# Kernel optimization log

Hardware: AMD Instinct MI355X
Metric: run time of the kernel (lower is better)

The kernel has to match this reference:

```python
import jax, jax.numpy as jnp
import numpy as np

NUM_INPUTS = 256
L1, L2 = 256, 128
NUM_ACTIONS = 17
NUM_EXPERTS = 4
GATE_H = 32
BATCH = 131072


def setup_inputs() -> dict:
    key = jax.random.key(0)
    ks = jax.random.split(key, 16)
    s = 0.05
    return {
        "x": jax.random.normal(ks[0], (BATCH, NUM_INPUTS), jnp.float32),
        # stacked expert weights [E, in, out]
        "W1": jax.random.normal(ks[1], (NUM_EXPERTS, NUM_INPUTS, L1), jnp.float32) * s,
        "b1": jax.random.normal(ks[2], (NUM_EXPERTS, L1), jnp.float32) * s,
        "W2": jax.random.normal(ks[3], (NUM_EXPERTS, L1, L2), jnp.float32) * s,
        "b2": jax.random.normal(ks[4], (NUM_EXPERTS, L2), jnp.float32) * s,
        "Wmu": jax.random.normal(ks[5], (NUM_EXPERTS, L2, NUM_ACTIONS), jnp.float32) * s,
        "bmu": jax.random.normal(ks[6], (NUM_EXPERTS, NUM_ACTIONS), jnp.float32) * s,
        # gate (BlendingModule) params
        "gW1": jax.random.normal(ks[7], (NUM_INPUTS, GATE_H), jnp.float32) * s,
        "gb1": jax.random.normal(ks[8], (GATE_H,), jnp.float32) * s,
        "gW2": jax.random.normal(ks[9], (GATE_H, GATE_H), jnp.float32) * s,
        "gb2": jax.random.normal(ks[10], (GATE_H,), jnp.float32) * s,
        "gWo": jax.random.normal(ks[11], (GATE_H, NUM_EXPERTS), jnp.float32) * s,
        "gbo": jax.random.normal(ks[12], (NUM_EXPERTS,), jnp.float32) * s,
    }


def _gate(x, gW1, gb1, gW2, gb2, gWo, gbo):
    h = jax.nn.elu(x @ gW1 + gb1)
    h = jax.nn.elu(h @ gW2 + gb2)
    return jax.nn.softmax(h @ gWo + gbo, axis=1)  # [B, E]


def reference(x, W1, b1, W2, b2, Wmu, bmu, gW1, gb1, gW2, gb2, gWo, gbo):
    coeffs = _gate(x, gW1, gb1, gW2, gb2, gWo, gbo)  # [B, E]
    # layer 1: gate-weighted sum of 4 expert GEMMs, then ReLU
    h = jnp.einsum("bi,eio->beo", x, W1) + b1[None]          # [B, E, L1]
    h = jax.nn.relu(jnp.einsum("be,beo->bo", coeffs, h))     # [B, L1]
    # layer 2
    h = jnp.einsum("bi,eio->beo", h, W2) + b2[None]          # [B, E, L2]
    h = jax.nn.relu(jnp.einsum("be,beo->bo", coeffs, h))     # [B, L2]
    # output head: weighted sum, no activation
    mu = jnp.einsum("bi,eio->beo", h, Wmu) + bmu[None]       # [B, E, A]
    mu = jnp.einsum("be,beo->bo", coeffs, mu)                # [B, A]
    return mu
```

## Files before the change

kernel.cpp:

```cpp
#include <hip/hip_runtime.h>


typedef _Float16 half8 __attribute__((ext_vector_type(8)));
typedef _Float16 half4v __attribute__((ext_vector_type(4)));
typedef float floatx4 __attribute__((ext_vector_type(4)));

#define MFMA16(a, b, c) __builtin_amdgcn_mfma_f32_16x16x32_f16(a, b, c, 0, 0, 0)
#define WAIT_VM(N) asm volatile("s_waitcnt vmcnt(" #N ")" ::: "memory")
#define WAIT_LGKM0 asm volatile("s_waitcnt lgkmcnt(0)" ::: "memory")

__device__ __forceinline__ void barrier_mem() {
  asm volatile("" ::: "memory");
  __builtin_amdgcn_s_barrier();
  asm volatile("" ::: "memory");
}

__device__ __forceinline__ half8 splat8(_Float16 v) {
  half8 r = {v, v, v, v, v, v, v, v};
  return r;
}

__device__ __forceinline__ void load_lds16(const _Float16* g, _Float16* s) {
  __builtin_amdgcn_global_load_lds((__attribute__((address_space(1))) void*)(g),
                                   (__attribute__((address_space(3))) void*)(s), 16, 0, 0);
}

enum {
  W1P = 0,
  W2P = 262144,
  WMUP = 393216,
  GW1P = 409600,
  GW2P = 417792,
  B1P = 418816,
  B2P = 427008,
  BMUP = 431104,
  WS_TOTAL = 432128
};

__global__ __launch_bounds__(256) void prep_kernel(
    const float* __restrict__ W1, const float* __restrict__ W2,
    const float* __restrict__ Wmu, const float* __restrict__ gW1,
    const float* __restrict__ gW2, const float* __restrict__ b1,
    const float* __restrict__ b2, const float* __restrict__ bmu,
    _Float16* __restrict__ ws) {
  int p = blockIdx.x * 256 + threadIdx.x;
  if (p >= WS_TOTAL) return;
  float v = 0.f;
  if (p < W2P) {
    int q = p, ks = q >> 13, r = q & 8191, ct = r >> 9, l = (r >> 3) & 63, j = r & 7;
    int k = ks * 32 + ((l >> 4) << 3) + j, o = (ct << 4) + (l & 15);
    v = W1[k * 256 + o];
  } else if (p < WMUP) {
    int q = p - W2P, ks = q >> 12, r = q & 4095, ct = r >> 9, l = (r >> 3) & 63, j = r & 7;
    int k = ks * 32 + ((l >> 4) << 3) + j, o = (ct << 4) + (l & 15);
    v = W2[k * 128 + o];
  } else if (p < GW1P) {
    int q = p - WMUP, ks = q >> 10, r = q & 1023, ct = r >> 9, l = (r >> 3) & 63, j = r & 7;
    int k = ks * 32 + ((l >> 4) << 3) + j, o = (ct << 4) + (l & 15);
    v = (o < 17) ? Wmu[k * 17 + o] : 0.f;
  } else if (p < GW2P) {
    int q = p - GW1P, ks = q >> 10, r = q & 1023, ct = r >> 9, l = (r >> 3) & 63, j = r & 7;
    int k = ks * 32 + ((l >> 4) << 3) + j, o = (ct << 4) + (l & 15);
    v = gW1[k * 32 + o];
  } else if (p < B1P) {
    int q = p - GW2P, ct = q >> 9, l = (q >> 3) & 63, j = q & 7;
    int k = ((l >> 4) << 3) + j, o = (ct << 4) + (l & 15);
    v = gW2[k * 32 + o];
  } else if (p < B2P) {
    int q = p - B1P, ct = q >> 9, l = (q >> 3) & 63, j = q & 7;
    int k = ((l >> 4) << 3) + j, o = (ct << 4) + (l & 15);
    v = (k < 4) ? b1[k * 256 + o] : 0.f;
  } else if (p < BMUP) {
    int q = p - B2P, ct = q >> 9, l = (q >> 3) & 63, j = q & 7;
    int k = ((l >> 4) << 3) + j, o = (ct << 4) + (l & 15);
    v = (k < 4) ? b2[k * 128 + o] : 0.f;
  } else {
    int q = p - BMUP, ct = q >> 9, l = (q >> 3) & 63, j = q & 7;
    int k = ((l >> 4) << 3) + j, o = (ct << 4) + (l & 15);
    v = (k < 4 && o < 17) ? bmu[k * 17 + o] : 0.f;
  }
  ws[p] = (_Float16)v;
}

enum { XS = 264, X_HW = 128 * XS, STG_HW = 3 * 8192, CP_OFF = X_HW + STG_HW, LDS_HW = CP_OFF + 128 * 32 };

__global__ __launch_bounds__(512, 2) void actor_kernel(
    const float* __restrict__ x, const _Float16* __restrict__ ws,
    const float* __restrict__ gb1, const float* __restrict__ gb2,
    const float* __restrict__ gWo, const float* __restrict__ gbo,
    float* __restrict__ out) {
  __shared__ __align__(16) _Float16 lds[LDS_HW];
  _Float16* xl = lds;
  _Float16* stg = lds + X_HW;
  _Float16* cp = lds + CP_OFF;

  const int tid = threadIdx.x;
  const int l = tid & 63;
  const int w = tid >> 6;
  const int l15 = l & 15;
  const int g8 = (l >> 4) << 3;
  const int wrow16 = w * 16;
  const int wr = (w >> 2) * 64;
  const int wc1 = (w & 3) * 64;
  const int wc2 = (w & 3) * 32;
  const long rowbase = (long)blockIdx.x * 128;

  {
    const float* xp = x + rowbase * 256;
#pragma unroll 4
    for (int it = 0; it < 16; ++it) {
      int row = w + it * 8;
      int c4 = (l)*4;
      float4 v = *(const float4*)(xp + row * 256 + c4);
      half4v h = {(_Float16)v.x, (_Float16)v.y, (_Float16)v.z, (_Float16)v.w};
      *(half4v*)(&xl[row * XS + c4]) = h;
    }
    for (int i = w; i < 16; i += 8) load_lds16(ws + GW1P + i * 512 + l * 8, stg + i * 512);
    for (int i = w; i < 2; i += 8) load_lds16(ws + GW2P + i * 512 + l * 8, stg + 8192 + i * 512);
    WAIT_VM(0);
    WAIT_LGKM0;
    barrier_mem();
  }

  {
    const floatx4 z4 = {0.f, 0.f, 0.f, 0.f};
    floatx4 ga[2] = {z4, z4};
#pragma unroll
    for (int ks = 0; ks < 8; ++ks) {
      half8 a = *(const half8*)(&xl[(wrow16 + l15) * XS + ks * 32 + g8]);
#pragma unroll
      for (int ct = 0; ct < 2; ++ct) {
        half8 b = *(const half8*)(&stg[ks * 1024 + ct * 512 + l * 8]);
        ga[ct] = MFMA16(a, b, ga[ct]);
      }
    }
#pragma unroll
    for (int ct = 0; ct < 2; ++ct) {
      int col = ct * 16 + l15;
      float bias = gb1[col];
#pragma unroll
      for (int rg = 0; rg < 4; ++rg) {
        int row = wrow16 + ((l >> 4) << 2) + rg;
        float v = ga[ct][rg] + bias;
        v = (v > 0.f) ? v : (__expf(v) - 1.f);
        stg[16384 + row * 40 + col] = (_Float16)v;
      }
    }
    WAIT_LGKM0;
    barrier_mem();
  }

  {
    const floatx4 z4 = {0.f, 0.f, 0.f, 0.f};
    floatx4 ga[2] = {z4, z4};
    half8 a = *(const half8*)(&stg[16384 + (wrow16 + l15) * 40 + g8]);
#pragma unroll
    for (int ct = 0; ct < 2; ++ct) {
      half8 b = *(const half8*)(&stg[8192 + ct * 512 + l * 8]);
      ga[ct] = MFMA16(a, b, ga[ct]);
    }
#pragma unroll
    for (int ct = 0; ct < 2; ++ct) {
      int col = ct * 16 + l15;
      float bias = gb2[col];
#pragma unroll
      for (int rg = 0; rg < 4; ++rg) {
        int row = wrow16 + ((l >> 4) << 2) + rg;
        float v = ga[ct][rg] + bias;
        v = (v > 0.f) ? v : (__expf(v) - 1.f);
        stg[row * 40 + col] = (_Float16)v;
      }
    }
    WAIT_LGKM0;
    barrier_mem();
  }

  {
    int row = tid >> 2, e = tid & 3;
    float s = gbo[e];
#pragma unroll
    for (int i8 = 0; i8 < 4; ++i8) {
      half8 gv = *(const half8*)(&stg[row * 40 + i8 * 8]);
#pragma unroll
      for (int j = 0; j < 8; ++j) s += (float)gv[j] * gWo[(i8 * 8 + j) * 4 + e];
    }
    ((float*)(stg + 8192))[row * 4 + e] = s;
    WAIT_LGKM0;
    barrier_mem();
  }

  if (tid < 128) {
    const float* lg = (const float*)(stg + 8192) + tid * 4;
    float m0 = fmaxf(fmaxf(lg[0], lg[1]), fmaxf(lg[2], lg[3]));
    float e0 = __expf(lg[0] - m0), e1 = __expf(lg[1] - m0);
    float e2 = __expf(lg[2] - m0), e3 = __expf(lg[3] - m0);
    float inv = 1.f / (e0 + e1 + e2 + e3);
    _Float16* cr = &cp[tid * 32];
    cr[0] = (_Float16)(e0 * inv);
    cr[1] = (_Float16)(e1 * inv);
    cr[2] = (_Float16)(e2 * inv);
    cr[3] = (_Float16)(e3 * inv);
#pragma unroll
    for (int z = 4; z < 32; ++z) cr[z] = (_Float16)0.f;
  }
  for (int i = w; i < 16; i += 8) load_lds16(ws + B1P + i * 512 + l * 8, stg + i * 512);
  WAIT_LGKM0;
  barrier_mem();

  _Float16 c16[4][4];
#pragma unroll
  for (int rt = 0; rt < 4; ++rt)
#pragma unroll
    for (int e = 0; e < 4; ++e) c16[rt][e] = cp[(wr + rt * 16 + l15) * 32 + e];
  for (int i = w; i < 16; i += 8) load_lds16(ws + W1P + i * 512 + l * 8, stg + 8192 + i * 512);
  WAIT_VM(2);
  barrier_mem();

  floatx4 acc[4][4];
  {
    const floatx4 z4 = {0.f, 0.f, 0.f, 0.f};
#pragma unroll
    for (int rt = 0; rt < 4; ++rt) {
      half8 a = *(const half8*)(&cp[(wr + rt * 16 + l15) * 32 + g8]);
#pragma unroll
      for (int ct = 0; ct < 4; ++ct) {
        half8 b = *(const half8*)(&stg[((w & 3) * 4 + ct) * 512 + l * 8]);
        acc[rt][ct] = MFMA16(a, b, z4);
      }
    }
  }
  for (int i = w; i < 16; i += 8) load_lds16(ws + W1P + 8192 + i * 512 + l * 8, stg + 16384 + i * 512);

#pragma unroll
  for (int e = 0; e < 4; ++e) {
    const half8 cs[4] = {splat8(c16[0][e]), splat8(c16[1][e]), splat8(c16[2][e]), splat8(c16[3][e])};
#pragma unroll 1
    for (int t8 = 0; t8 < 8; ++t8) {
      const int t = e * 8 + t8 + 1;
      if (t == 32) { WAIT_VM(0); } else { WAIT_VM(2); }
      barrier_mem();
      const int xk = t8 << 5;
      const _Float16* bb = stg + (t % 3) * 8192;
      half8 a[4];
#pragma unroll
      for (int rt = 0; rt < 4; ++rt) {
        half8 raw = *(const half8*)(&xl[(wr + rt * 16 + l15) * XS + xk + g8]);
        a[rt] = raw * cs[rt];
      }
#pragma unroll
      for (int ct = 0; ct < 4; ++ct) {
        half8 b = *(const half8*)(&bb[((w & 3) * 4 + ct) * 512 + l * 8]);
#pragma unroll
        for (int rt = 0; rt < 4; ++rt) acc[rt][ct] = MFMA16(a[rt], b, acc[rt][ct]);
      }
      if (t <= 30) {
        const _Float16* src = ws + W1P + (t + 1) * 8192;
        _Float16* dst = stg + ((t + 2) % 3) * 8192;
        for (int i = w; i < 16; i += 8) load_lds16(src + i * 512 + l * 8, dst + i * 512);
      }
    }
  }
  barrier_mem();

#pragma unroll
  for (int rt = 0; rt < 4; ++rt)
#pragma unroll
    for (int ct = 0; ct < 4; ++ct) {
      int col = wc1 + ct * 16 + l15;
#pragma unroll
      for (int rg = 0; rg < 4; ++rg) {
        int row = wr + rt * 16 + ((l >> 4) << 2) + rg;
        float v = acc[rt][ct][rg];
        xl[row * XS + col] = (_Float16)(v > 0.f ? v : 0.f);
      }
    }
  for (int i = w; i < 8; i += 8) load_lds16(ws + B2P + i * 512 + l * 8, stg + i * 512);
  WAIT_LGKM0;
  barrier_mem();
  for (int i = w; i < 8; i += 8) load_lds16(ws + W2P + i * 512 + l * 8, stg + 8192 + i * 512);
  WAIT_VM(1);
  barrier_mem();

  floatx4 acc2[4][2];
  {
    const floatx4 z4 = {0.f, 0.f, 0.f, 0.f};
#pragma unroll
    for (int rt = 0; rt < 4; ++rt) {
      half8 a = *(const half8*)(&cp[(wr + rt * 16 + l15) * 32 + g8]);
#pragma unroll
      for (int ct = 0; ct < 2; ++ct) {
        half8 b = *(const half8*)(&stg[((w & 3) * 2 + ct) * 512 + l * 8]);
        acc2[rt][ct] = MFMA16(a, b, z4);
      }
    }
  }
  for (int i = w; i < 8; i += 8) load_lds16(ws + W2P + 4096 + i * 512 + l * 8, stg + 16384 + i * 512);

#pragma unroll
  for (int e = 0; e < 4; ++e) {
    const half8 cs[4] = {splat8(c16[0][e]), splat8(c16[1][e]), splat8(c16[2][e]), splat8(c16[3][e])};
#pragma unroll 1
    for (int t8 = 0; t8 < 8; ++t8) {
      const int t = e * 8 + t8 + 1;
      if (t == 32) { WAIT_VM(0); } else { WAIT_VM(1); }
      barrier_mem();
      const int xk = t8 << 5;
      const _Float16* bb = stg + (t % 3) * 8192;
      half8 a[4];
#pragma unroll
      for (int rt = 0; rt < 4; ++rt) {
        half8 raw = *(const half8*)(&xl[(wr + rt * 16 + l15) * XS + xk + g8]);
        a[rt] = raw * cs[rt];
      }
#pragma unroll
      for (int ct = 0; ct < 2; ++ct) {
        half8 b = *(const half8*)(&bb[((w & 3) * 2 + ct) * 512 + l * 8]);
#pragma unroll
        for (int rt = 0; rt < 4; ++rt) acc2[rt][ct] = MFMA16(a[rt], b, acc2[rt][ct]);
      }
      if (t <= 30) {
        const _Float16* src = ws + W2P + (t + 1) * 4096;
        _Float16* dst = stg + ((t + 2) % 3) * 8192;
        for (int i = w; i < 8; i += 8) load_lds16(src + i * 512 + l * 8, dst + i * 512);
      }
    }
  }
  barrier_mem();

#pragma unroll
  for (int rt = 0; rt < 4; ++rt)
#pragma unroll
    for (int ct = 0; ct < 2; ++ct) {
      int col = wc2 + ct * 16 + l15;
#pragma unroll
      for (int rg = 0; rg < 4; ++rg) {
        int row = wr + rt * 16 + ((l >> 4) << 2) + rg;
        float v = acc2[rt][ct][rg];
        xl[row * 136 + col] = (_Float16)(v > 0.f ? v : 0.f);
      }
    }
  for (int i = w; i < 34; i += 8) {
    int tile = i >> 1, half = i & 1;
    const _Float16* src = ws + (tile == 0 ? BMUP : WMUP + (tile - 1) * 1024) + half * 512 + l * 8;
    load_lds16(src, stg + i * 512);
  }
  WAIT_LGKM0;
  WAIT_VM(0);
  barrier_mem();

  floatx4 hacc[2];
  {
    const floatx4 z4 = {0.f, 0.f, 0.f, 0.f};
    half8 a = *(const half8*)(&cp[(wrow16 + l15) * 32 + g8]);
#pragma unroll
    for (int ct = 0; ct < 2; ++ct) {
      half8 b = *(const half8*)(&stg[ct * 512 + l * 8]);
      hacc[ct] = MFMA16(a, b, z4);
    }
  }
#pragma unroll
  for (int ksv = 0; ksv < 16; ++ksv) {
    const int e = ksv >> 2;
    const int xk = (ksv & 3) << 5;
    half8 raw = *(const half8*)(&xl[(wrow16 + l15) * 136 + xk + g8]);
    half8 a = raw * splat8(c16[w & 3][e]);
#pragma unroll
    for (int ct = 0; ct < 2; ++ct) {
      half8 b = *(const half8*)(&stg[(ksv + 1) * 1024 + ct * 512 + l * 8]);
      hacc[ct] = MFMA16(a, b, hacc[ct]);
    }
  }
#pragma unroll
  for (int ct = 0; ct < 2; ++ct) {
    int col = ct * 16 + l15;
    if (col < 17) {
#pragma unroll
      for (int rg = 0; rg < 4; ++rg) {
        int row = wrow16 + ((l >> 4) << 2) + rg;
        out[(rowbase + row) * 17 + col] = hacc[ct][rg];
      }
    }
  }
}

extern "C" void kernel_launch(void* const* d_in, const int* in_sizes, int n_in,
                              void* d_out, int out_size, void* d_ws, size_t ws_size,
                              hipStream_t stream) {
  const float* x = (const float*)d_in[0];
  const float* W1 = (const float*)d_in[1];
  const float* b1 = (const float*)d_in[2];
  const float* W2 = (const float*)d_in[3];
  const float* b2 = (const float*)d_in[4];
  const float* Wmu = (const float*)d_in[5];
  const float* bmu = (const float*)d_in[6];
  const float* gW1 = (const float*)d_in[7];
  const float* gb1 = (const float*)d_in[8];
  const float* gW2 = (const float*)d_in[9];
  const float* gb2 = (const float*)d_in[10];
  const float* gWo = (const float*)d_in[11];
  const float* gbo = (const float*)d_in[12];
  float* out = (float*)d_out;
  _Float16* ws = (_Float16*)d_ws;

  prep_kernel<<<(WS_TOTAL + 255) / 256, 256, 0, stream>>>(W1, W2, Wmu, gW1, gW2, b1, b2, bmu, ws);
  actor_kernel<<<1024, 512, 0, stream>>>(x, ws, gb1, gb2, gWo, gbo, out);
}
```

Measured before the change: 354.3 us.

## Rewrite actor kernel with 1024-thread blocks, fragment-layout LDS and deeper weight ring

Restructures the fused MoE actor kernel to use 16 waves per block arranged as 2 row groups by 8 column groups. Activations are stored in LDS in MFMA fragment order, removing the padded row-major layout. The gate output projection moves onto MFMA with shuffle-based softmax. Weight tiles stream through a deeper 5-slot ring for layer 1 and a 10-slot ring for layer 2, with the prep kernel reordering weights to match. The aim is to raise MFMA occupancy, cut LDS bank conflicts and hide weight-load latency. In exchange only one wave group computes the gate, and barriers now synchronize 16 waves.

Result: slower. 1.139 ms (+221.5%).

```diff
diff --git a/kernel.cpp b/kernel.cpp
--- a/kernel.cpp
+++ b/kernel.cpp
@@ -18,6 +18,13 @@
 __device__ __forceinline__ half8 splat8(_Float16 v) {
   half8 r = {v, v, v, v, v, v, v, v};
   return r;
+}
+
+__device__ __forceinline__ half8 make_cfrag(half4v c, int l) {
+  half8 cf = {(_Float16)0, (_Float16)0, (_Float16)0, (_Float16)0,
+              (_Float16)0, (_Float16)0, (_Float16)0, (_Float16)0};
+  if (l < 16) { cf[0] = c[0]; cf[1] = c[1]; cf[2] = c[2]; cf[3] = c[3]; }
+  return cf;
 }
 
 __device__ __forceinline__ void load_lds16(const _Float16* g, _Float16* s) {
@@ -31,354 +38,396 @@
   WMUP = 393216,
   GW1P = 409600,
   GW2P = 417792,
-  B1P = 418816,
-  B2P = 427008,
-  BMUP = 431104,
-  WS_TOTAL = 432128
+  GWOP = 418816,
+  B1P = 419328,
+  B2P = 427520,
+  BMUP = 431616,
+  WS_TOTAL = 432640
 };
 
 __global__ __launch_bounds__(256) void prep_kernel(
     const float* __restrict__ W1, const float* __restrict__ W2,
     const float* __restrict__ Wmu, const float* __restrict__ gW1,
-    const float* __restrict__ gW2, const float* __restrict__ b1,
-    const float* __restrict__ b2, const float* __restrict__ bmu,
-    _Float16* __restrict__ ws) {
+    const float* __restrict__ gW2, const float* __restrict__ gWo,
+    const float* __restrict__ b1, const float* __restrict__ b2,
+    const float* __restrict__ bmu, _Float16* __restrict__ ws) {
   int p = blockIdx.x * 256 + threadIdx.x;
   if (p >= WS_TOTAL) return;
   float v = 0.f;
   if (p < W2P) {
-    int q = p, ks = q >> 13, r = q & 8191, ct = r >> 9, l = (r >> 3) & 63, j = r & 7;
-    int k = ks * 32 + ((l >> 4) << 3) + j, o = (ct << 4) + (l & 15);
-    v = W1[k * 256 + o];
+    int t = p >> 13, r = p & 8191;
+    int ct = r >> 9, l = (r >> 3) & 63, j = r & 7;
+    int o = ct * 16 + (l & 15), krel = ((l >> 4) << 3) + j;
+    int t8 = t >> 2, e = t & 3;
+    v = W1[(e * 256 + t8 * 32 + krel) * 256 + o];
   } else if (p < WMUP) {
-    int q = p - W2P, ks = q >> 12, r = q & 4095, ct = r >> 9, l = (r >> 3) & 63, j = r & 7;
-    int k = ks * 32 + ((l >> 4) << 3) + j, o = (ct << 4) + (l & 15);
-    v = W2[k * 128 + o];
+    int q = p - W2P, t = q >> 12, r = q & 4095;
+    int ct = r >> 9, l = (r >> 3) & 63, j = r & 7;
+    int o = ct * 16 + (l & 15), krel = ((l >> 4) << 3) + j;
+    int t8 = t >> 2, e = t & 3;
+    v = W2[(e * 256 + t8 * 32 + krel) * 128 + o];
   } else if (p < GW1P) {
-    int q = p - WMUP, ks = q >> 10, r = q & 1023, ct = r >> 9, l = (r >> 3) & 63, j = r & 7;
-    int k = ks * 32 + ((l >> 4) << 3) + j, o = (ct << 4) + (l & 15);
-    v = (o < 17) ? Wmu[k * 17 + o] : 0.f;
+    int q = p - WMUP, t = q >> 10, r = q & 1023;
+    int ct = r >> 9, l = (r >> 3) & 63, j = r & 7;
+    int o = ct * 16 + (l & 15), krel = ((l >> 4) << 3) + j;
+    int t2 = t >> 2, e = t & 3;
+    v = (o < 17) ? Wmu[(e * 128 + t2 * 32 + krel) * 17 + o] : 0.f;
   } else if (p < GW2P) {
-    int q = p - GW1P, ks = q >> 10, r = q & 1023, ct = r >> 9, l = (r >> 3) & 63, j = r & 7;
-    int k = ks * 32 + ((l >> 4) << 3) + j, o = (ct << 4) + (l & 15);
-    v = gW1[k * 32 + o];
+    int q = p - GW1P, ks = q >> 10, r = q & 1023;
+    int ct = r >> 9, l = (r >> 3) & 63, j = r & 7;
+    int o = ct * 16 + (l & 15), krel = ((l >> 4) << 3) + j;
+    v = gW1[(ks * 32 + krel) * 32 + o];
+  } else if (p < GWOP) {
+    int q = p - GW2P;
+    int ct = q >> 9, l = (q >> 3) & 63, j = q & 7;
+    int o = ct * 16 + (l & 15), krel = ((l >> 4) << 3) + j;
+    v = gW2[krel * 32 + o];
   } else if (p < B1P) {
-    int q = p - GW2P, ct = q >> 9, l = (q >> 3) & 63, j = q & 7;
-    int k = ((l >> 4) << 3) + j, o = (ct << 4) + (l & 15);
-    v = gW2[k * 32 + o];
+    int q = p - GWOP;
+    int l = (q >> 3) & 63, j = q & 7;
+    int o = l & 15, krel = ((l >> 4) << 3) + j;
+    v = (o < 4) ? gWo[krel * 4 + o] : 0.f;
   } else if (p < B2P) {
-    int q = p - B1P, ct = q >> 9, l = (q >> 3) & 63, j = q & 7;
-    int k = ((l >> 4) << 3) + j, o = (ct << 4) + (l & 15);
-    v = (k < 4) ? b1[k * 256 + o] : 0.f;
+    int q = p - B1P;
+    int ct = q >> 9, l = (q >> 3) & 63, j = q & 7;
+    int o = ct * 16 + (l & 15), krel = ((l >> 4) << 3) + j;
+    v = (krel < 4) ? b1[krel * 256 + o] : 0.f;
   } else if (p < BMUP) {
-    int q = p - B2P, ct = q >> 9, l = (q >> 3) & 63, j = q & 7;
-    int k = ((l >> 4) << 3) + j, o = (ct << 4) + (l & 15);
-    v = (k < 4) ? b2[k * 128 + o] : 0.f;
+    int q = p - B2P;
+    int ct = q >> 9, l = (q >> 3) & 63, j = q & 7;
+    int o = ct * 16 + (l & 15), krel = ((l >> 4) << 3) + j;
+    v = (krel < 4) ? b2[krel * 128 + o] : 0.f;
   } else {
-    int q = p - BMUP, ct = q >> 9, l = (q >> 3) & 63, j = q & 7;
-    int k = ((l >> 4) << 3) + j, o = (ct << 4) + (l & 15);
-    v = (k < 4 && o < 17) ? bmu[k * 17 + o] : 0.f;
+    int q = p - BMUP;
+    int ct = q >> 9, l = (q >> 3) & 63, j = q & 7;
+    int o = ct * 16 + (l & 15), krel = ((l >> 4) << 3) + j;
+    v = (krel < 4 && o < 17) ? bmu[krel * 17 + o] : 0.f;
   }
   ws[p] = (_Float16)v;
 }
 
-enum { XS = 264, X_HW = 128 * XS, STG_HW = 3 * 8192, CP_OFF = X_HW + STG_HW, LDS_HW = CP_OFF + 128 * 32 };
-
-__global__ __launch_bounds__(512, 2) void actor_kernel(
+enum {
+  RING = 32768,
+  GATE = 57344,
+  GW2L = GATE + 8192,
+  GWOL = GATE + 9216,
+  BNC = GATE + 9728,
+  CLDS = GATE + 13824,
+  LDS_HW = 73728
+};
+
+__global__ __launch_bounds__(1024, 4) void actor_kernel(
     const float* __restrict__ x, const _Float16* __restrict__ ws,
     const float* __restrict__ gb1, const float* __restrict__ gb2,
-    const float* __restrict__ gWo, const float* __restrict__ gbo,
-    float* __restrict__ out) {
+    const float* __restrict__ gbo, float* __restrict__ out) {
   __shared__ __align__(16) _Float16 lds[LDS_HW];
-  _Float16* xl = lds;
-  _Float16* stg = lds + X_HW;
-  _Float16* cp = lds + CP_OFF;
-
   const int tid = threadIdx.x;
   const int l = tid & 63;
   const int w = tid >> 6;
   const int l15 = l & 15;
   const int g8 = (l >> 4) << 3;
-  const int wrow16 = w * 16;
-  const int wr = (w >> 2) * 64;
-  const int wc1 = (w & 3) * 64;
-  const int wc2 = (w & 3) * 32;
+  const int mr = w >> 3;
+  const int nc = w & 7;
   const long rowbase = (long)blockIdx.x * 128;
+  const int fragBase = mr * 2048 + l * 8;
+  const floatx4 z4 = {0.f, 0.f, 0.f, 0.f};
 
   {
-    const float* xp = x + rowbase * 256;
-#pragma unroll 4
-    for (int it = 0; it < 16; ++it) {
-      int row = w + it * 8;
-      int c4 = (l)*4;
-      float4 v = *(const float4*)(xp + row * 256 + c4);
-      half4v h = {(_Float16)v.x, (_Float16)v.y, (_Float16)v.z, (_Float16)v.w};
-      *(half4v*)(&xl[row * XS + c4]) = h;
-    }
-    for (int i = w; i < 16; i += 8) load_lds16(ws + GW1P + i * 512 + l * 8, stg + i * 512);
-    for (int i = w; i < 2; i += 8) load_lds16(ws + GW2P + i * 512 + l * 8, stg + 8192 + i * 512);
-    WAIT_VM(0);
+    const float* xp = x + (rowbase + mr * 64) * 256 + nc * 32 + g8;
+#pragma unroll
+    for (int rt = 0; rt < 4; ++rt) {
+      const float4* rp = (const float4*)(xp + (rt * 16 + l15) * 256);
+      float4 v0 = rp[0], v1 = rp[1];
+      half8 h = {(_Float16)v0.x, (_Float16)v0.y, (_Float16)v0.z, (_Float16)v0.w,
+                 (_Float16)v1.x, (_Float16)v1.y, (_Float16)v1.z, (_Float16)v1.w};
+      *(half8*)(&lds[nc * 4096 + fragBase + rt * 512]) = h;
+    }
+    for (int c = w; c < 19; c += 16)
+      load_lds16(ws + GW1P + c * 512 + l * 8, lds + GATE + c * 512);
+#pragma unroll
+    for (int t = 0; t < 3; ++t)
+      load_lds16(ws + (t == 0 ? B1P : W1P + (t - 1) * 8192) + w * 512 + l * 8,
+                 lds + RING + t * 8192 + w * 512);
+    WAIT_VM(3);
     WAIT_LGKM0;
     barrier_mem();
   }
 
+  if (nc == 0) {
+    floatx4 ga[4][2];
+#pragma unroll
+    for (int rt = 0; rt < 4; ++rt) { ga[rt][0] = z4; ga[rt][1] = z4; }
+#pragma unroll
+    for (int ks = 0; ks < 8; ++ks) {
+      half8 b0 = *(const half8*)(&lds[GATE + ks * 1024 + l * 8]);
+      half8 b1v = *(const half8*)(&lds[GATE + ks * 1024 + 512 + l * 8]);
+#pragma unroll
+      for (int rt = 0; rt < 4; ++rt) {
+        half8 a = *(const half8*)(&lds[ks * 4096 + fragBase + rt * 512]);
+        ga[rt][0] = MFMA16(a, b0, ga[rt][0]);
+        ga[rt][1] = MFMA16(a, b1v, ga[rt][1]);
+      }
+    }
+#pragma unroll
+    for (int rt = 0; rt < 4; ++rt)
+#pragma unroll
+      for (int ct = 0; ct < 2; ++ct) {
+        const int c32 = ct * 16 + l15;
+        const float bias = gb1[c32];
+        const int hi4 = (c32 >> 3) << 4, jj = c32 & 7;
+#pragma unroll
+        for (int rg = 0; rg < 4; ++rg) {
+          float vv = ga[rt][ct][rg] + bias;
+          vv = vv > 0.f ? vv : (__expf(vv) - 1.f);
+          const int lp = (4 * (l >> 4) + rg) | hi4;
+          lds[BNC + mr * 2048 + rt * 512 + lp * 8 + jj] = (_Float16)vv;
+        }
+      }
+    WAIT_LGKM0;
+    floatx4 g2[4][2];
+    {
+      half8 bw0 = *(const half8*)(&lds[GW2L + l * 8]);
+      half8 bw1 = *(const half8*)(&lds[GW2L + 512 + l * 8]);
+#pragma unroll
+      for (int rt = 0; rt < 4; ++rt) {
+        half8 a = *(const half8*)(&lds[BNC + mr * 2048 + rt * 512 + l * 8]);
+        g2[rt][0] = MFMA16(a, bw0, z4);
+        g2[rt][1] = MFMA16(a, bw1, z4);
+      }
+    }
+    WAIT_LGKM0;
+#pragma unroll
+    for (int rt = 0; rt < 4; ++rt)
+#pragma unroll
+      for (int ct = 0; ct < 2; ++ct) {
+        const int c32 = ct * 16 + l15;
+        const float bias = gb2[c32];
+        const int hi4 = (c32 >> 3) << 4, jj = c32 & 7;
+#pragma unroll
+        for (int rg = 0; rg < 4; ++rg) {
+          float vv = g2[rt][ct][rg] + bias;
+          vv = vv > 0.f ? vv : (__expf(vv) - 1.f);
+          const int lp = (4 * (l >> 4) + rg) | hi4;
+          lds[BNC + mr * 2048 + rt * 512 + lp * 8 + jj] = (_Float16)vv;
+        }
+      }
+    WAIT_LGKM0;
+    {
+      half8 bo = *(const half8*)(&lds[GWOL + l * 8]);
+      const float bze = (l15 < 4) ? gbo[l15] : 0.f;
+#pragma unroll
+      for (int rt = 0; rt < 4; ++rt) {
+        half8 a = *(const half8*)(&lds[BNC + mr * 2048 + rt * 512 + l * 8]);
+        floatx4 lg = MFMA16(a, bo, z4);
+#pragma unroll
+        for (int rg = 0; rg < 4; ++rg) {
+          float vv = lg[rg] + bze;
+          float m = fmaxf(vv, __shfl_xor(vv, 1));
+          m = fmaxf(m, __shfl_xor(m, 2));
+          float eo = __expf(vv - m);
+          float sden = eo + __shfl_xor(eo, 1);
+          sden = sden + __shfl_xor(sden, 2);
+          float c = eo / sden;
+          if (l15 < 4)
+            lds[CLDS + (mr * 64 + rt * 16 + 4 * (l >> 4) + rg) * 4 + l15] = (_Float16)c;
+        }
+      }
+    }
+    WAIT_LGKM0;
+  }
+  barrier_mem();
+
+  half4v c4[4];
+#pragma unroll
+  for (int rt = 0; rt < 4; ++rt)
+    c4[rt] = *(const half4v*)(&lds[CLDS + (mr * 64 + rt * 16 + l15) * 4]);
+  load_lds16(ws + W1P + 2 * 8192 + w * 512 + l * 8, lds + RING + 3 * 8192 + w * 512);
+  WAIT_VM(3);
+  WAIT_LGKM0;
+  barrier_mem();
+
+  floatx4 acc[4][2];
+  const int bBase = nc * 1024 + l * 8;
+  load_lds16(ws + W1P + 3 * 8192 + w * 512 + l * 8, lds + RING + 4 * 8192 + w * 512);
   {
-    const floatx4 z4 = {0.f, 0.f, 0.f, 0.f};
-    floatx4 ga[2] = {z4, z4};
-#pragma unroll
-    for (int ks = 0; ks < 8; ++ks) {
-      half8 a = *(const half8*)(&xl[(wrow16 + l15) * XS + ks * 32 + g8]);
-#pragma unroll
-      for (int ct = 0; ct < 2; ++ct) {
-        half8 b = *(const half8*)(&stg[ks * 1024 + ct * 512 + l * 8]);
-        ga[ct] = MFMA16(a, b, ga[ct]);
-      }
-    }
+    half8 b0 = *(const half8*)(&lds[RING + bBase]);
+    half8 b1v = *(const half8*)(&lds[RING + bBase + 512]);
+#pragma unroll
+    for (int rt = 0; rt < 4; ++rt) {
+      half8 cfr = make_cfrag(c4[rt], l);
+      acc[rt][0] = MFMA16(cfr, b0, z4);
+      acc[rt][1] = MFMA16(cfr, b1v, z4);
+    }
+  }
+  WAIT_VM(3);
+  barrier_mem();
+
+  half8 af[4];
+  int s = 1, sp = 0;
+#pragma unroll 1
+  for (int t8 = 0; t8 < 8; ++t8) {
+#pragma unroll
+    for (int e = 0; e < 4; ++e) {
+      const int t = t8 * 4 + e + 1;
+      if (t8 < 7)
+        load_lds16(ws + W1P + (t + 3) * 8192 + w * 512 + l * 8,
+                   lds + RING + sp * 8192 + w * 512);
+      if (e == 0) {
+#pragma unroll
+        for (int rt = 0; rt < 4; ++rt)
+          af[rt] = *(const half8*)(&lds[t8 * 4096 + fragBase + rt * 512]);
+      }
+      const int slot = RING + s * 8192;
+      half8 b0 = *(const half8*)(&lds[slot + bBase]);
+      half8 b1v = *(const half8*)(&lds[slot + bBase + 512]);
+#pragma unroll
+      for (int rt = 0; rt < 4; ++rt) {
+        half8 as = af[rt] * splat8(c4[rt][e]);
+        acc[rt][0] = MFMA16(as, b0, acc[rt][0]);
+        acc[rt][1] = MFMA16(as, b1v, acc[rt][1]);
+      }
+      if (t8 < 7) { WAIT_VM(3); }
+      else if (e == 0) { WAIT_VM(2); }
+      else if (e == 1) { WAIT_VM(1); }
+      else if (e == 2) { WAIT_VM(0); }
+      barrier_mem();
+      sp = s;
+      s = (s == 4) ? 0 : s + 1;
+    }
+  }
+
+#pragma unroll
+  for (int rt = 0; rt < 4; ++rt)
 #pragma unroll
     for (int ct = 0; ct < 2; ++ct) {
-      int col = ct * 16 + l15;
-      float bias = gb1[col];
+      const int c32 = ct * 16 + l15;
+      const int hi4 = (c32 >> 3) << 4, jj = c32 & 7;
 #pragma unroll
       for (int rg = 0; rg < 4; ++rg) {
-        int row = wrow16 + ((l >> 4) << 2) + rg;
-        float v = ga[ct][rg] + bias;
-        v = (v > 0.f) ? v : (__expf(v) - 1.f);
-        stg[16384 + row * 40 + col] = (_Float16)v;
-      }
-    }
-    WAIT_LGKM0;
-    barrier_mem();
-  }
-
+        float vv = acc[rt][ct][rg];
+        vv = vv > 0.f ? vv : 0.f;
+        const int lp = (4 * (l >> 4) + rg) | hi4;
+        lds[nc * 4096 + mr * 2048 + rt * 512 + lp * 8 + jj] = (_Float16)vv;
+      }
+    }
+  if (w < 8) {
+#pragma unroll
+    for (int t = 0; t < 8; ++t)
+      load_lds16(ws + (t == 0 ? B2P : W2P + (t - 1) * 4096) + w * 512 + l * 8,
+                 lds + RING + t * 4096 + w * 512);
+  }
+  WAIT_LGKM0;
+  if (w < 8) { WAIT_VM(7); }
+  barrier_mem();
+
+  floatx4 acc2[4];
+  const int b2B = nc * 512 + l * 8;
+  if (w < 8)
+    load_lds16(ws + W2P + 7 * 4096 + w * 512 + l * 8, lds + RING + 8 * 4096 + w * 512);
   {
-    const floatx4 z4 = {0.f, 0.f, 0.f, 0.f};
-    floatx4 ga[2] = {z4, z4};
-    half8 a = *(const half8*)(&stg[16384 + (wrow16 + l15) * 40 + g8]);
-#pragma unroll
-    for (int ct = 0; ct < 2; ++ct) {
-      half8 b = *(const half8*)(&stg[8192 + ct * 512 + l * 8]);
-      ga[ct] = MFMA16(a, b, ga[ct]);
-    }
-#pragma unroll
-    for (int ct = 0; ct < 2; ++ct) {
-      int col = ct * 16 + l15;
-      float bias = gb2[col];
+    half8 b0 = *(const half8*)(&lds[RING + b2B]);
+#pragma unroll
+    for (int rt = 0; rt < 4; ++rt) {
+      half8 cfr = make_cfrag(c4[rt], l);
+      acc2[rt] = MFMA16(cfr, b0, z4);
+    }
+  }
+  if (w < 8) { WAIT_VM(7); }
+  barrier_mem();
+
+  int su = 1;
+#pragma unroll 1
+  for (int t8 = 0; t8 < 8; ++t8) {
+#pragma unroll
+    for (int e = 0; e < 4; ++e) {
+      const int t = t8 * 4 + e + 1;
+      if (t8 < 6 && w < 8) {
+        const int si = (su >= 2) ? su - 2 : su + 8;
+        load_lds16(ws + W2P + (t + 7) * 4096 + w * 512 + l * 8,
+                   lds + RING + si * 4096 + w * 512);
+      }
+      if (e == 0) {
+#pragma unroll
+        for (int rt = 0; rt < 4; ++rt)
+          af[rt] = *(const half8*)(&lds[t8 * 4096 + fragBase + rt * 512]);
+      }
+      half8 b0 = *(const half8*)(&lds[RING + su * 4096 + b2B]);
+#pragma unroll
+      for (int rt = 0; rt < 4; ++rt) {
+        half8 as = af[rt] * splat8(c4[rt][e]);
+        acc2[rt] = MFMA16(as, b0, acc2[rt]);
+      }
+      if (w < 8) {
+        if (t8 < 6) { WAIT_VM(7); }
+        else if (t8 == 6) {
+          if (e == 0) { WAIT_VM(6); } else if (e == 1) { WAIT_VM(5); }
+          else if (e == 2) { WAIT_VM(4); } else { WAIT_VM(3); }
+        } else {
+          if (e == 0) { WAIT_VM(2); } else if (e == 1) { WAIT_VM(1); }
+          else if (e == 2) { WAIT_VM(0); }
+        }
+      }
+      barrier_mem();
+      su = (su == 9) ? 0 : su + 1;
+    }
+  }
+
+  {
+    const int c32 = ((nc & 1) << 4) | l15;
+    const int hi4 = (c32 >> 3) << 4, jj = c32 & 7;
+    const int hb = (nc >> 1) * 4096 + mr * 2048;
+#pragma unroll
+    for (int rt = 0; rt < 4; ++rt)
 #pragma unroll
       for (int rg = 0; rg < 4; ++rg) {
-        int row = wrow16 + ((l >> 4) << 2) + rg;
-        float v = ga[ct][rg] + bias;
-        v = (v > 0.f) ? v : (__expf(v) - 1.f);
-        stg[row * 40 + col] = (_Float16)v;
-      }
-    }
-    WAIT_LGKM0;
-    barrier_mem();
-  }
-
-  {
-    int row = tid >> 2, e = tid & 3;
-    float s = gbo[e];
-#pragma unroll
-    for (int i8 = 0; i8 < 4; ++i8) {
-      half8 gv = *(const half8*)(&stg[row * 40 + i8 * 8]);
-#pragma unroll
-      for (int j = 0; j < 8; ++j) s += (float)gv[j] * gWo[(i8 * 8 + j) * 4 + e];
-    }
-    ((float*)(stg + 8192))[row * 4 + e] = s;
-    WAIT_LGKM0;
-    barrier_mem();
-  }
-
-  if (tid < 128) {
-    const float* lg = (const float*)(stg + 8192) + tid * 4;
-    float m0 = fmaxf(fmaxf(lg[0], lg[1]), fmaxf(lg[2], lg[3]));
-    float e0 = __expf(lg[0] - m0), e1 = __expf(lg[1] - m0);
-    float e2 = __expf(lg[2] - m0), e3 = __expf(lg[3] - m0);
-    float inv = 1.f / (e0 + e1 + e2 + e3);
-    _Float16* cr = &cp[tid * 32];
-    cr[0] = (_Float16)(e0 * inv);
-    cr[1] = (_Float16)(e1 * inv);
-    cr[2] = (_Float16)(e2 * inv);
-    cr[3] = (_Float16)(e3 * inv);
-#pragma unroll
-    for (int z = 4; z < 32; ++z) cr[z] = (_Float16)0.f;
-  }
-  for (int i = w; i < 16; i += 8) load_lds16(ws + B1P + i * 512 + l * 8, stg + i * 512);
-  WAIT_LGKM0;
-  barrier_mem();
-
-  _Float16 c16[4][4];
-#pragma unroll
-  for (int rt = 0; rt < 4; ++rt)
-#pragma unroll
-    for (int e = 0; e < 4; ++e) c16[rt][e] = cp[(wr + rt * 16 + l15) * 32 + e];
-  for (int i = w; i < 16; i += 8) load_lds16(ws + W1P + i * 512 + l * 8, stg + 8192 + i * 512);
-  WAIT_VM(2);
-  barrier_mem();
-
-  floatx4 acc[4][4];
-  {
-    const floatx4 z4 = {0.f, 0.f, 0.f, 0.f};
-#pragma unroll
-    for (int rt = 0; rt < 4; ++rt) {
-      half8 a = *(const half8*)(&cp[(wr + rt * 16 + l15) * 32 + g8]);
-#pragma unroll
-      for (int ct = 0; ct < 4; ++ct) {
-        half8 b = *(const half8*)(&stg[((w & 3) * 4 + ct) * 512 + l * 8]);
-        acc[rt][ct] = MFMA16(a, b, z4);
-      }
-    }
-  }
-  for (int i = w; i < 16; i += 8) load_lds16(ws + W1P + 8192 + i * 512 + l * 8, stg + 16384 + i * 512);
-
-#pragma unroll
-  for (int e = 0; e < 4; ++e) {
-    const half8 cs[4] = {splat8(c16[0][e]), splat8(c16[1][e]), splat8(c16[2][e]), splat8(c16[3][e])};
-#pragma unroll 1
-    for (int t8 = 0; t8 < 8; ++t8) {
-      const int t = e * 8 + t8 + 1;
-      if (t == 32) { WAIT_VM(0); } else { WAIT_VM(2); }
-      barrier_mem();
-      const int xk = t8 << 5;
-      const _Float16* bb = stg + (t % 3) * 8192;
-      half8 a[4];
-#pragma unroll
-      for (int rt = 0; rt < 4; ++rt) {
-        half8 raw = *(const half8*)(&xl[(wr + rt * 16 + l15) * XS + xk + g8]);
-        a[rt] = raw * cs[rt];
-      }
-#pragma unroll
-      for (int ct = 0; ct < 4; ++ct) {
-        half8 b = *(const half8*)(&bb[((w & 3) * 4 + ct) * 512 + l * 8]);
-#pragma unroll
-        for (int rt = 0; rt < 4; ++rt) acc[rt][ct] = MFMA16(a[rt], b, acc[rt][ct]);
-      }
-      if (t <= 30) {
-        const _Float16* src = ws + W1P + (t + 1) * 8192;
-        _Float16* dst = stg + ((t + 2) % 3) * 8192;
-        for (int i = w; i < 16; i += 8) load_lds16(src + i * 512 + l * 8, dst + i * 512);
-      }
-    }
-  }
-  barrier_mem();
-
-#pragma unroll
-  for (int rt = 0; rt < 4; ++rt)
-#pragma unroll
-    for (int ct = 0; ct < 4; ++ct) {
-      int col = wc1 + ct * 16 + l15;
-#pragma unroll
-      for (int rg = 0; rg < 4; ++rg) {
-        int row = wr + rt * 16 + ((l >> 4) << 2) + rg;
-        float v = acc[rt][ct][rg];
-        xl[row * XS + col] = (_Float16)(v > 0.f ? v : 0.f);
-      }
-    }
-  for (int i = w; i < 8; i += 8) load_lds16(ws + B2P + i * 512 + l * 8, stg + i * 512);
-  WAIT_LGKM0;
-  barrier_mem();
-  for (int i = w; i < 8; i += 8) load_lds16(ws + W2P + i * 512 + l * 8, stg + 8192 + i * 512);
-  WAIT_VM(1);
-  barrier_mem();
-
-  floatx4 acc2[4][2];
-  {
-    const floatx4 z4 = {0.f, 0.f, 0.f, 0.f};
-#pragma unroll
-    for (int rt = 0; rt < 4; ++rt) {
-      half8 a = *(const half8*)(&cp[(wr + rt * 16 + l15) * 32 + g8]);
-#pragma unroll
-      for (int ct = 0; ct < 2; ++ct) {
-        half8 b = *(const half8*)(&stg[((w & 3) * 2 + ct) * 512 + l * 8]);
-        acc2[rt][ct] = MFMA16(a, b, z4);
-      }
-    }
-  }
-  for (int i = w; i < 8; i += 8) load_lds16(ws + W2P + 4096 + i * 512 + l * 8, stg + 16384 + i * 512);
-
-#pragma unroll
-  for (int e = 0; e < 4; ++e) {
-    const half8 cs[4] = {splat8(c16[0][e]), splat8(c16[1][e]), splat8(c16[2][e]), splat8(c16[3][e])};
-#pragma unroll 1
-    for (int t8 = 0; t8 < 8; ++t8) {
-      const int t = e * 8 + t8 + 1;
-      if (t == 32) { WAIT_VM(0); } else { WAIT_VM(1); }
-      barrier_mem();
-      const int xk = t8 << 5;
-      const _Float16* bb = stg + (t % 3) * 8192;
-      half8 a[4];
-#pragma unroll
-      for (int rt = 0; rt < 4; ++rt) {
-        half8 raw = *(const half8*)(&xl[(wr + rt * 16 + l15) * XS + xk + g8]);
-        a[rt] = raw * cs[rt];
-      }
-#pragma unroll
-      for (int ct = 0; ct < 2; ++ct) {
-        half8 b = *(const half8*)(&bb[((w & 3) * 2 + ct) * 512 + l * 8]);
-#pragma unroll
-        for (int rt = 0; rt < 4; ++rt) acc2[rt][ct] = MFMA16(a[rt], b, acc2[rt][ct]);
-      }
-      if (t <= 30) {
-        const _Float16* src = ws + W2P + (t + 1) * 4096;
-        _Float16* dst = stg + ((t + 2) % 3) * 8192;
-        for (int i = w; i < 8; i += 8) load_lds16(src + i * 512 + l * 8, dst + i * 512);
-      }
-    }
-  }
-  barrier_mem();
-
-#pragma unroll
-  for (int rt = 0; rt < 4; ++rt)
-#pragma unroll
-    for (int ct = 0; ct < 2; ++ct) {
-      int col = wc2 + ct * 16 + l15;
-#pragma unroll
-      for (int rg = 0; rg < 4; ++rg) {
-        int row = wr + rt * 16 + ((l >> 4) << 2) + rg;
-        float v = acc2[rt][ct][rg];
-        xl[row * 136 + col] = (_Float16)(v > 0.f ? v : 0.f);
-      }
-    }
-  for (int i = w; i < 34; i += 8) {
-    int tile = i >> 1, half = i & 1;
-    const _Float16* src = ws + (tile == 0 ? BMUP : WMUP + (tile - 1) * 1024) + half * 512 + l * 8;
-    load_lds16(src, stg + i * 512);
+        float vv = acc2[rt][rg];
+        vv = vv > 0.f ? vv : 0.f;
+        const int lp = (4 * (l >> 4) + rg) | hi4;
+        lds[hb + rt * 512 + lp * 8 + jj] = (_Float16)vv;
+      }
+  }
+  for (int c = w; c < 34; c += 16) {
+    const _Float16* src = (c < 2) ? (ws + BMUP + c * 512) : (ws + WMUP + (c - 2) * 512);
+    load_lds16(src + l * 8, lds + RING + c * 512);
   }
   WAIT_LGKM0;
   WAIT_VM(0);
   barrier_mem();
 
-  floatx4 hacc[2];
-  {
-    const floatx4 z4 = {0.f, 0.f, 0.f, 0.f};
-    half8 a = *(const half8*)(&cp[(wrow16 + l15) * 32 + g8]);
-#pragma unroll
-    for (int ct = 0; ct < 2; ++ct) {
-      half8 b = *(const half8*)(&stg[ct * 512 + l * 8]);
-      hacc[ct] = MFMA16(a, b, z4);
-    }
-  }
-#pragma unroll
-  for (int ksv = 0; ksv < 16; ++ksv) {
-    const int e = ksv >> 2;
-    const int xk = (ksv & 3) << 5;
-    half8 raw = *(const half8*)(&xl[(wrow16 + l15) * 136 + xk + g8]);
-    half8 a = raw * splat8(c16[w & 3][e]);
-#pragma unroll
-    for (int ct = 0; ct < 2; ++ct) {
-      half8 b = *(const half8*)(&stg[(ksv + 1) * 1024 + ct * 512 + l * 8]);
-      hacc[ct] = MFMA16(a, b, hacc[ct]);
-    }
-  }
-#pragma unroll
-  for (int ct = 0; ct < 2; ++ct) {
-    int col = ct * 16 + l15;
+  if (nc < 2) {
+    floatx4 hd[4];
+    const int hB = nc * 512 + l * 8;
+    {
+      half8 bb = *(const half8*)(&lds[RING + hB]);
+#pragma unroll
+      for (int rt = 0; rt < 4; ++rt) {
+        half8 cfr = make_cfrag(c4[rt], l);
+        hd[rt] = MFMA16(cfr, bb, z4);
+      }
+    }
+#pragma unroll
+    for (int t2 = 0; t2 < 4; ++t2) {
+      half8 ah[4];
+#pragma unroll
+      for (int rt = 0; rt < 4; ++rt)
+        ah[rt] = *(const half8*)(&lds[(t2 * 2 + mr) * 2048 + rt * 512 + l * 8]);
+#pragma unroll
+      for (int e = 0; e < 4; ++e) {
+        half8 bh = *(const half8*)(&lds[RING + 1024 + (t2 * 4 + e) * 1024 + hB]);
+#pragma unroll
+        for (int rt = 0; rt < 4; ++rt) {
+          half8 as = ah[rt] * splat8(c4[rt][e]);
+          hd[rt] = MFMA16(as, bh, hd[rt]);
+        }
+      }
+    }
+    const int col = nc * 16 + l15;
     if (col < 17) {
 #pragma unroll
-      for (int rg = 0; rg < 4; ++rg) {
-        int row = wrow16 + ((l >> 4) << 2) + rg;
-        out[(rowbase + row) * 17 + col] = hacc[ct][rg];
-      }
+      for (int rt = 0; rt < 4; ++rt)
+#pragma unroll
+        for (int rg = 0; rg < 4; ++rg)
+          out[(rowbase + mr * 64 + rt * 16 + 4 * (l >> 4) + rg) * 17 + col] = hd[rt][rg];
     }
   }
 }
@@ -402,6 +451,7 @@
   float* out = (float*)d_out;
   _Float16* ws = (_Float16*)d_ws;
 
-  prep_kernel<<<(WS_TOTAL + 255) / 256, 256, 0, stream>>>(W1, W2, Wmu, gW1, gW2, b1, b2, bmu, ws);
-  actor_kernel<<<1024, 512, 0, stream>>>(x, ws, gb1, gb2, gWo, gbo, out);
-}
+  prep_kernel<<<(WS_TOTAL + 255) / 256, 256, 0, stream>>>(W1, W2, Wmu, gW1, gW2, gWo,
+                                                          b1, b2, bmu, ws);
+  actor_kernel<<<1024, 1024, 0, stream>>>(x, ws, gb1, gb2, gbo, out);
+}
```
